# Optimization experiments

Hardware: AMD Instinct MI355X
Metric: run time of the kernel (lower is better)

## Reference

```python
import jax, jax.numpy as jnp
import numpy as np

IMAGE_SIZE = 256
DET = int(IMAGE_SIZE * 2 ** 0.5 + 0.5)  # 362 detector bins (diagonal coverage)
US = 4
N_ACQ = 45                     # acquired views: 0,4,...,176 degrees
N_FULL = (N_ACQ - 1) * US + 1  # 177 full (upsampled) views


def setup_inputs() -> dict:
    key = jax.random.key(0)
    k1, k2 = jax.random.split(key)
    x_source = jax.random.normal(k1, (2, 1, IMAGE_SIZE, IMAGE_SIZE), jnp.float32)
    s_target = jax.random.normal(k2, (2, 1, DET, N_ACQ), jnp.float32)
    theta_acq = np.arange(0, 180, 4, dtype=np.float64)  # 45 acquired angles
    segs = [np.linspace(theta_acq[i], theta_acq[i + 1], US + 1)[:-1] for i in range(N_ACQ - 1)]
    theta_full = np.concatenate(segs + [theta_acq[-1:]]).astype(np.float32)  # [177]
    acq_idx = (np.arange(N_ACQ) * US).astype(np.int32)  # positions of acquired angles in theta_full
    return {"x_source": x_source, "s_target": s_target,
            "thetas_deg": jnp.asarray(theta_full), "acq_idx": jnp.asarray(acq_idx)}


def bilinear_gather(img, xs, ys):
    # img: [B,C,H,W]; xs, ys: pixel coords [A,det,det]; zero outside the image.
    H, W = img.shape[-2], img.shape[-1]
    x0 = jnp.floor(xs); y0 = jnp.floor(ys)
    wx = xs - x0; wy = ys - y0
    x0i = x0.astype(jnp.int32); y0i = y0.astype(jnp.int32)

    def get(yi, xi):
        valid = (xi >= 0) & (xi < W) & (yi >= 0) & (yi < H)
        v = img[:, :, jnp.clip(yi, 0, H - 1), jnp.clip(xi, 0, W - 1)]  # [B,C,A,det,det]
        return jnp.where(valid, v, 0.0)

    return (get(y0i, x0i) * (1 - wy) * (1 - wx)
            + get(y0i, x0i + 1) * (1 - wy) * wx
            + get(y0i + 1, x0i) * wy * (1 - wx)
            + get(y0i + 1, x0i + 1) * wy * wx)


def radon(x, thetas_rad, det):
    # Ray-sum projection: sino[theta, t] = sum_s image(t*cos - s*sin, t*sin + s*cos)
    B, C, H, W = x.shape
    t = jnp.arange(det, dtype=x.dtype) - (det - 1) / 2.0  # centered detector/ray coord
    cos = jnp.cos(thetas_rad)[:, None, None]
    sin = jnp.sin(thetas_rad)[:, None, None]
    T = t[None, :, None]; S = t[None, None, :]
    xs = T * cos - S * sin + (W - 1) / 2.0  # [A,det,det]
    ys = T * sin + S * cos + (H - 1) / 2.0
    return bilinear_gather(x, xs, ys).sum(-1)  # [B,C,A,det]


def ramp_filter(size):
    # skimage/pytorch_radon style ramp built from its real-space kernel
    n = np.concatenate([np.arange(1, size // 2 + 1, 2), np.arange(size // 2 - 1, 0, -2)])
    f = np.zeros(size)
    f[0] = 0.25
    f[1::2] = -1.0 / (np.pi * n) ** 2
    return jnp.asarray(2 * np.real(np.fft.fft(f)), dtype=jnp.float32)


def fbp(sino, thetas_rad, image_size):
    # Filtered back-projection. sino: [B,C,det,A]
    B, C, det, A = sino.shape
    pad = max(64, int(2 ** np.ceil(np.log2(2 * det))))
    filt = ramp_filter(pad)  # [pad]
    sp = jnp.pad(sino, ((0, 0), (0, 0), (0, pad - det), (0, 0)))
    sf = jnp.fft.ifft(jnp.fft.fft(sp, axis=2) * filt[None, None, :, None], axis=2).real
    sf = jnp.transpose(sf[:, :, :det, :], (0, 1, 3, 2)).astype(sino.dtype)  # [B,C,A,det]
    g = jnp.arange(image_size, dtype=sino.dtype) - (image_size - 1) / 2.0
    cos = jnp.cos(thetas_rad); sin = jnp.sin(thetas_rad)
    # detector coordinate hit by each pixel, per angle: t = x*cos + y*sin
    t = (cos[:, None, None] * g[None, None, :]
         + sin[:, None, None] * g[None, :, None] + (det - 1) / 2.0)  # [A,H,W]
    t = t.reshape(A, -1)
    t0 = jnp.floor(t)
    w = t - t0
    t0i = t0.astype(jnp.int32)
    aidx = jnp.arange(A)[:, None]

    def samp(ti):
        valid = (ti >= 0) & (ti < det)
        return jnp.where(valid, sf[:, :, aidx, jnp.clip(ti, 0, det - 1)], 0.0)  # [B,C,A,HW]

    v = samp(t0i) * (1 - w) + samp(t0i + 1) * w
    reco = v.sum(2) * (jnp.pi / (2 * A))
    return reco.reshape(B, C, image_size, image_size)


def reference(x_source, s_target, thetas_deg, acq_idx):
    th = thetas_deg * (jnp.pi / 180.0)
    s = radon(x_source, th, DET)          # [B,C,A,det]
    s = jnp.transpose(s, (0, 1, 3, 2))    # [B,C,det,A] -- angle axis last, as in the module
    # masked data-consistency update: acquired columns become (target - predicted)
    s = s.at[..., acq_idx].set(s_target - s[..., acq_idx])
    return fbp(s, th, IMAGE_SIZE)
```

## Files before the change

### kernel.cpp

```cpp
#include <hip/hip_runtime.h>
#include <math.h>

#define IMG   256
#define NFULL 177
#define DETN  362
#define NACQ  45
#define PAD   1024

#define SINO_OFF 0
#define SF_OFF   131072

#define TTILE  32
#define HALF_T 180.5f
#define SEGL   32
#define TILE_SEG 2548

__constant__ const int kByOrder[12] = {5, 6, 4, 7, 3, 8, 2, 9, 1, 10, 0, 11};

__device__ __forceinline__ void gload16(const float* g, float* l) {
    __builtin_amdgcn_global_load_lds(
        (const __attribute__((address_space(1))) void*)g,
        (__attribute__((address_space(3))) void*)l, 16, 0, 0);
}

template<int P>
__device__ __forceinline__ float radon_core(
    const float* __restrict__ img,
    float* tile,
    const float c, const float s,
    const float xbase, const float ybase,
    const float xAB_mn, const float yAB_mn, const float yAB_mx,
    const int SloB, const int ShiB, const int tid)
{
    constexpr int W4   = P / 4;
    constexpr int HMAX = TILE_SEG / P;
    const int ts   = tid & 7;
    const int wid  = tid >> 6;
    const int lane = tid & 63;

    auto window = [&](int Sseg) -> int4 {
        const float sv0 = (float)Sseg - HALF_T;
        const float sv1 = sv0 + (float)(SEGL - 1);
        const float xmn = xAB_mn - sv1 * s;
        const float ya  = sv0 * c, yb = sv1 * c;
        const float ymn = yAB_mn + fminf(ya, yb);
        const float ymx = yAB_mx + fmaxf(ya, yb);
        const int ix0  = (int)floorf(xmn) - 1;
        const int iy0  = (int)floorf(ymn) - 1;
        const int ix0a = ix0 & ~3;
        const int h    = min((int)floorf(ymx) + 3 - iy0, HMAX);
        const int inter = (ix0a >= 0) & (iy0 >= 0) &
                          (ix0a + P <= IMG) & (iy0 + h <= IMG);
        return make_int4(ix0a, iy0, h, inter);
    };

    auto stage = [&](const int4 wp, float* tb) {
        const int total4 = W4 * wp.z;
        const int nfull  = total4 & ~63;
        if (wp.w) {
            const float* __restrict__ src = img + wp.y * IMG + wp.x;
            for (int f0 = wid * 64; f0 < nfull; f0 += 256) {
                const int f  = f0 + lane;
                const int r  = f / W4;
                const int c4 = f - r * W4;
                gload16(src + r * IMG + (c4 << 2), tb + (f0 << 2));
            }
            const int f = nfull + tid;
            if (f < total4) {
                const int r  = f / W4;
                const int c4 = f - r * W4;
                gload16(src + r * IMG + (c4 << 2), tb + (nfull << 2));
            }
        } else {
            for (int f = tid; f < total4; f += 256) {
                const int r  = f / W4;
                const int c4 = f - r * W4;
                const int gy = wp.y + r;
                const int gx = wp.x + (c4 << 2);
                const bool ok = ((unsigned)gy < (unsigned)IMG) &
                                ((unsigned)gx <= (unsigned)(IMG - 4));
                float4 v = make_float4(0.f, 0.f, 0.f, 0.f);
                if (ok) v = *(const float4*)(img + gy * IMG + gx);
                *(float4*)(tb + (f << 2)) = v;
            }
        }
    };

    float val = 0.0f;
    if (SloB >= ShiB) return val;

    int4 wp = window(SloB);
    stage(wp, tile);
    __syncthreads();

    int cur = 0;
    for (int Sseg = SloB; Sseg < ShiB; Sseg += SEGL) {
        const int Snext = Sseg + SEGL;
        int4 wpn = wp;
        if (Snext < ShiB) {
            wpn = window(Snext);
            stage(wpn, tile + (cur ^ 1) * TILE_SEG);
        }

        const float* __restrict__ tb = tile + cur * TILE_SEG;
        const float xoff = xbase - (float)wp.x;
        const float yoff = ybase - (float)wp.y;
        const int Send = min(Snext, ShiB);

        auto samp = [&](float sval) {
            const float xs  = fmaf(-sval, s, xoff);
            const float ys  = fmaf(sval, c, yoff);
            const float x0f = floorf(xs);
            const float y0f = floorf(ys);
            const float wx  = xs - x0f;
            const float wy  = ys - y0f;
            const int base = (int)fmaf(y0f, (float)P, x0f);
            const float v00 = tb[base];
            const float v01 = tb[base + 1];
            const float v10 = tb[base + P];
            const float v11 = tb[base + P + 1];
            const float h0 = fmaf(wx, v01 - v00, v00);
            const float h1 = fmaf(wx, v11 - v10, v10);
            val += fmaf(wy, h1 - h0, h0);
        };

        if (Send - Sseg == SEGL) {
            const float s0 = (float)(Sseg + ts) - HALF_T;
            #pragma unroll
            for (int u = 0; u < SEGL / 8; ++u) samp(s0 + (float)(8 * u));
        } else {
            for (int S = Sseg + ts; S < Send; S += 8) samp((float)S - HALF_T);
        }
        __syncthreads();
        wp = wpn;
        cur ^= 1;
    }
    return val;
}

__global__ __launch_bounds__(256, 8) void radon_kernel(
    const float* __restrict__ x,
    const float* __restrict__ thetas,
    float* __restrict__ sino)
{
    const int blk = blockIdx.x;
    const int b = blk / NFULL;
    const int a = blk - b * NFULL;
    const int T0 = kByOrder[blockIdx.y] * TTILE;
    const int tid = threadIdx.x;
    const int ts = tid & 7;
    const int tt = tid >> 3;
    const int T = T0 + tt;

    __shared__ __align__(16) float tile[2 * TILE_SEG];
    __shared__ int sRange[2];
    __shared__ int sSel;

    const float th = thetas[a] * (float)(M_PI / 180.0);
    const float c = cosf(th);
    const float s = sinf(th);
    const float cx = (IMG - 1) * 0.5f;
    const float cy = (IMG - 1) * 0.5f;
    const float Tc = (float)T - HALF_T;
    const float xbase = Tc * c + cx;
    const float ybase = Tc * s + cy;

    float lo = -1e30f, hi = 1e30f;
    bool empty = (T >= DETN);
    {   const float aa = -s;
        if (aa > 1e-5f)       { lo = fmaxf(lo, (-1.0f - xbase) / aa); hi = fminf(hi, (256.0f - xbase) / aa); }
        else if (aa < -1e-5f) { lo = fmaxf(lo, (256.0f - xbase) / aa); hi = fminf(hi, (-1.0f - xbase) / aa); }
        else if (xbase <= -1.0f || xbase >= 256.0f) empty = true;
    }
    {   const float aa = c;
        if (aa > 1e-5f)       { lo = fmaxf(lo, (-1.0f - ybase) / aa); hi = fminf(hi, (256.0f - ybase) / aa); }
        else if (aa < -1e-5f) { lo = fmaxf(lo, (256.0f - ybase) / aa); hi = fminf(hi, (-1.0f - ybase) / aa); }
        else if (ybase <= -1.0f || ybase >= 256.0f) empty = true;
    }
    lo = fmaxf(lo, -200.0f);
    hi = fminf(hi, 200.0f);
    int Slo = max(0, (int)floorf(lo + HALF_T) - 1);
    int Shi = min(DETN, (int)floorf(hi + HALF_T) + 2);
    if (empty || Shi < Slo) { Slo = 0; Shi = 0; }

    if (tid == 0) { sRange[0] = DETN; sRange[1] = 0; }
    __syncthreads();
    if (Shi > Slo) { atomicMin(&sRange[0], Slo); atomicMax(&sRange[1], Shi); }

    if (tid < 64) {
        const int ltt = tid >> 3, lts = tid & 7;
        const float ac = fabsf(c), as = fabsf(s);
        const float span = 31.f * (ac + as);
        const int hm[5] = {57, 53, 49, 45, 42};
        int best = 2, bcost = 1 << 30;
        #pragma unroll
        for (int p = 0; p < 5; ++p) {
            const float Pf = 44.f + 4.f * (float)p;
            const float dT = s * Pf + c;
            const float dS = c * Pf - s;
            const int bank = (int)floorf((float)ltt * dT + (float)lts * dS + 0.5f) & 31;
            unsigned long long m = ~0ull;
            #pragma unroll
            for (int bit = 0; bit < 5; ++bit) {
                const unsigned long long bb = __ballot((bank >> bit) & 1);
                m &= ((bank >> bit) & 1) ? bb : ~bb;
            }
            int cnt = __popcll(m);
            #pragma unroll
            for (int d = 1; d < 64; d <<= 1) cnt = max(cnt, __shfl_xor(cnt, d, 64));
            const bool fit = (span <= Pf - 8.05f) && (span <= (float)hm[p] - 5.05f);
            if (fit && cnt < bcost) { bcost = cnt; best = p; }
        }
        if (tid == 0) sSel = best;
    }
    __syncthreads();
    const int SloB = sRange[0], ShiB = sRange[1];
    const int selv = sSel;

    const float TcA = (float)T0 - HALF_T;
    const float TcB = (float)(T0 + TTILE - 1) - HALF_T;
    const float xAB_mn = fminf(TcA * c + cx, TcB * c + cx);
    const float yAB_mn = fminf(TcA * s + cy, TcB * s + cy);
    const float yAB_mx = fmaxf(TcA * s + cy, TcB * s + cy);

    const float* __restrict__ img = x + b * IMG * IMG;

    float val;
    switch (selv) {
    case 0:  val = radon_core<44>(img, tile, c, s, xbase, ybase,
                                  xAB_mn, yAB_mn, yAB_mx, SloB, ShiB, tid); break;
    case 1:  val = radon_core<48>(img, tile, c, s, xbase, ybase,
                                  xAB_mn, yAB_mn, yAB_mx, SloB, ShiB, tid); break;
    case 2:  val = radon_core<52>(img, tile, c, s, xbase, ybase,
                                  xAB_mn, yAB_mn, yAB_mx, SloB, ShiB, tid); break;
    case 3:  val = radon_core<56>(img, tile, c, s, xbase, ybase,
                                  xAB_mn, yAB_mn, yAB_mx, SloB, ShiB, tid); break;
    default: val = radon_core<60>(img, tile, c, s, xbase, ybase,
                                  xAB_mn, yAB_mn, yAB_mx, SloB, ShiB, tid); break;
    }

    val += __shfl_xor(val, 1, 8);
    val += __shfl_xor(val, 2, 8);
    val += __shfl_xor(val, 4, 8);
    if (ts == 0 && T < DETN) {
        sino[(b * NFULL + a) * DETN + T] = val;
    }
}

__global__ __launch_bounds__(192) void dc_filter_kernel(
    const float* __restrict__ sino,
    const float* __restrict__ st,
    const int*   __restrict__ acq,
    float* __restrict__ sf)
{
    const int blk = blockIdx.x;
    const int b = blk / NFULL;
    const int a = blk - b * NFULL;
    const int tid = threadIdx.x;

    __shared__ float col[DETN];
    __shared__ float gf[PAD];

    const float SC = (float)(M_PI / (2.0 * NFULL));
    const float c0 = 0.5f * SC;
    for (int n = tid; n < PAD; n += 192) {
        float v = 0.0f;
        if (n & 1) {
            const int d = (n < PAD - n) ? n : (PAD - n);
            const float pd = (float)M_PI * (float)d;
            v = -2.0f / (pd * pd) * SC;
        }
        gf[n] = v;
    }

    int inv = -1;
    for (int i = 0; i < NACQ; ++i) {
        if (acq[i] == a) inv = i;
    }

    for (int m = tid; m < DETN; m += 192) {
        float val = sino[(b * NFULL + a) * DETN + m];
        if (inv >= 0) {
            val = st[(b * DETN + m) * NACQ + inv] - val;
        }
        col[m] = val;
    }
    __syncthreads();

    const int T = blockIdx.y * 181 + tid;
    if (tid < 181) {
        const int m0 = (T + 1) & 1;
        float acc = c0 * col[T];
        #pragma unroll 4
        for (int k = 0; k < 181; ++k) {
            const int m = m0 + 2 * k;
            acc += col[m] * gf[(T - m) & (PAD - 1)];
        }
        sf[(b * NFULL + a) * DETN + T] = acc;
    }
}

__global__ __launch_bounds__(256) void backproject_kernel(
    const float* __restrict__ sf,
    const float* __restrict__ thetas,
    float* __restrict__ out)
{
    __shared__ float cb[2 * NFULL];
    __shared__ float red[256];
    const int tid = threadIdx.x;
    const int lane  = tid & 63;
    const int phase = tid >> 6;
    const int pix = blockIdx.x * 64 + lane;
    const int b = pix >> 16;
    const int y = (pix >> 8) & 255;
    const int xq = pix & 255;
    const float gx = (float)xq - (IMG - 1) * 0.5f;
    const float gy = (float)y  - (IMG - 1) * 0.5f;

    for (int a = tid; a < NFULL; a += 256) {
        float th = thetas[a] * (float)(M_PI / 180.0);
        cb[2 * a]     = cosf(th);
        cb[2 * a + 1] = fmaf(sinf(th), gy, HALF_T);
    }
    __syncthreads();

    const float* __restrict__ sfb = sf + b * NFULL * DETN;

    float acc = 0.0f;
    #pragma unroll 4
    for (int a = phase; a < NFULL; a += 4) {
        const float cs = cb[2 * a];
        const float bs = cb[2 * a + 1];
        const float t = fmaf(cs, gx, bs);
        const float t0f = floorf(t);
        const float w = t - t0f;
        const float* row = sfb + a * DETN + (int)t0f;
        const float v0 = row[0];
        const float v1 = row[1];
        acc += v0 + w * (v1 - v0);
    }
    red[tid] = acc;
    __syncthreads();
    if (tid < 64) {
        out[blockIdx.x * 64 + tid] =
            red[tid] + red[tid + 64] + red[tid + 128] + red[tid + 192];
    }
}

extern "C" void kernel_launch(void* const* d_in, const int* in_sizes, int n_in,
                              void* d_out, int out_size, void* d_ws, size_t ws_size,
                              hipStream_t stream) {
    const float* x      = (const float*)d_in[0];
    const float* st     = (const float*)d_in[1];
    const float* thetas = (const float*)d_in[2];
    const int*   acq    = (const int*)d_in[3];
    float* out  = (float*)d_out;
    float* wsf  = (float*)d_ws;
    float* sino = wsf + SINO_OFF;
    float* sf   = wsf + SF_OFF;

    dim3 gA(2 * NFULL, 12);
    radon_kernel<<<gA, 256, 0, stream>>>(x, thetas, sino);
    dim3 gB(2 * NFULL, 2);
    dc_filter_kernel<<<gB, 192, 0, stream>>>(sino, st, acq, sf);
    backproject_kernel<<<(2 * IMG * IMG) / 64, 256, 0, stream>>>(sf, thetas, out);
}
```

Measured before the change: 126.8 us.

## Restructure radon kernel into per-wave 8-detector strips with wave-local LDS staging

```diff
diff --git a/kernel.cpp b/kernel.cpp
--- a/kernel.cpp
+++ b/kernel.cpp
@@ -10,12 +10,12 @@
 #define SINO_OFF 0
 #define SF_OFF   131072
 
-#define TTILE  32
 #define HALF_T 180.5f
 #define SEGL   32
-#define TILE_SEG 2548
-
-__constant__ const int kByOrder[12] = {5, 6, 4, 7, 3, 8, 2, 9, 1, 10, 0, 11};
+#define TILE_W 1276
+
+__constant__ const int kPairOrd[23] =
+    {11,10,12,9,13,8,14,7,15,6,16,5,17,4,18,3,19,2,20,1,21,0,22};
 
 __device__ __forceinline__ void gload16(const float* g, float* l) {
     __builtin_amdgcn_global_load_lds(
@@ -24,21 +24,20 @@
 }
 
 template<int P>
-__device__ __forceinline__ float radon_core(
+__device__ __forceinline__ float radon_strip(
     const float* __restrict__ img,
-    float* tile,
+    float* tb,
     const float c, const float s,
     const float xbase, const float ybase,
     const float xAB_mn, const float yAB_mn, const float yAB_mx,
-    const int SloB, const int ShiB, const int tid)
+    const int Slo, const int Shi, const int lane)
 {
     constexpr int W4   = P / 4;
-    constexpr int HMAX = TILE_SEG / P;
-    const int ts   = tid & 7;
-    const int wid  = tid >> 6;
-    const int lane = tid & 63;
-
-    auto window = [&](int Sseg) -> int4 {
+    constexpr int HMAX = TILE_W / P;
+    const int ts = lane & 7;
+    float val = 0.0f;
+
+    for (int Sseg = Slo; Sseg < Shi; Sseg += SEGL) {
         const float sv0 = (float)Sseg - HALF_T;
         const float sv1 = sv0 + (float)(SEGL - 1);
         const float xmn = xAB_mn - sv1 * s;
@@ -49,34 +48,33 @@
         const int iy0  = (int)floorf(ymn) - 1;
         const int ix0a = ix0 & ~3;
         const int h    = min((int)floorf(ymx) + 3 - iy0, HMAX);
-        const int inter = (ix0a >= 0) & (iy0 >= 0) &
-                          (ix0a + P <= IMG) & (iy0 + h <= IMG);
-        return make_int4(ix0a, iy0, h, inter);
-    };
-
-    auto stage = [&](const int4 wp, float* tb) {
-        const int total4 = W4 * wp.z;
+        const int total4 = W4 * h;
         const int nfull  = total4 & ~63;
-        if (wp.w) {
-            const float* __restrict__ src = img + wp.y * IMG + wp.x;
-            for (int f0 = wid * 64; f0 < nfull; f0 += 256) {
+        const bool interior = (ix0a >= 0) & (iy0 >= 0) &
+                              (ix0a + P <= IMG) & (iy0 + h <= IMG);
+
+        asm volatile("s_waitcnt lgkmcnt(0)" ::: "memory");
+
+        if (interior) {
+            const float* __restrict__ src = img + iy0 * IMG + ix0a;
+            for (int f0 = 0; f0 < nfull; f0 += 64) {
                 const int f  = f0 + lane;
                 const int r  = f / W4;
                 const int c4 = f - r * W4;
                 gload16(src + r * IMG + (c4 << 2), tb + (f0 << 2));
             }
-            const int f = nfull + tid;
+            const int f = nfull + lane;
             if (f < total4) {
                 const int r  = f / W4;
                 const int c4 = f - r * W4;
                 gload16(src + r * IMG + (c4 << 2), tb + (nfull << 2));
             }
         } else {
-            for (int f = tid; f < total4; f += 256) {
+            for (int f = lane; f < total4; f += 64) {
                 const int r  = f / W4;
                 const int c4 = f - r * W4;
-                const int gy = wp.y + r;
-                const int gx = wp.x + (c4 << 2);
+                const int gy = iy0 + r;
+                const int gx = ix0a + (c4 << 2);
                 const bool ok = ((unsigned)gy < (unsigned)IMG) &
                                 ((unsigned)gx <= (unsigned)(IMG - 4));
                 float4 v = make_float4(0.f, 0.f, 0.f, 0.f);
@@ -84,28 +82,12 @@
                 *(float4*)(tb + (f << 2)) = v;
             }
         }
-    };
-
-    float val = 0.0f;
-    if (SloB >= ShiB) return val;
-
-    int4 wp = window(SloB);
-    stage(wp, tile);
-    __syncthreads();
-
-    int cur = 0;
-    for (int Sseg = SloB; Sseg < ShiB; Sseg += SEGL) {
-        const int Snext = Sseg + SEGL;
-        int4 wpn = wp;
-        if (Snext < ShiB) {
-            wpn = window(Snext);
-            stage(wpn, tile + (cur ^ 1) * TILE_SEG);
-        }
-
-        const float* __restrict__ tb = tile + cur * TILE_SEG;
-        const float xoff = xbase - (float)wp.x;
-        const float yoff = ybase - (float)wp.y;
-        const int Send = min(Snext, ShiB);
+        asm volatile("s_waitcnt vmcnt(0) lgkmcnt(0)" ::: "memory");
+        __builtin_amdgcn_sched_barrier(0);
+
+        const float xoff = xbase - (float)ix0a;
+        const float yoff = ybase - (float)iy0;
+        const int Send = min(Sseg + SEGL, Shi);
 
         auto samp = [&](float sval) {
             const float xs  = fmaf(-sval, s, xoff);
@@ -131,14 +113,11 @@
         } else {
             for (int S = Sseg + ts; S < Send; S += 8) samp((float)S - HALF_T);
         }
-        __syncthreads();
-        wp = wpn;
-        cur ^= 1;
     }
     return val;
 }
 
-__global__ __launch_bounds__(256, 8) void radon_kernel(
+__global__ __launch_bounds__(128, 8) void radon_kernel(
     const float* __restrict__ x,
     const float* __restrict__ thetas,
     float* __restrict__ sino)
@@ -146,15 +125,16 @@
     const int blk = blockIdx.x;
     const int b = blk / NFULL;
     const int a = blk - b * NFULL;
-    const int T0 = kByOrder[blockIdx.y] * TTILE;
-    const int tid = threadIdx.x;
-    const int ts = tid & 7;
-    const int tt = tid >> 3;
-    const int T = T0 + tt;
-
-    __shared__ __align__(16) float tile[2 * TILE_SEG];
-    __shared__ int sRange[2];
-    __shared__ int sSel;
+    const int w    = threadIdx.x >> 6;
+    const int lane = threadIdx.x & 63;
+    const int sp   = kPairOrd[blockIdx.y] * 2 + w;
+    const int T0   = sp << 3;
+    const int tt   = lane >> 3;
+    const int ts   = lane & 7;
+    const int T    = T0 + tt;
+
+    __shared__ __align__(16) float tile[2][TILE_W];
+    float* tb = tile[w];
 
     const float th = thetas[a] * (float)(M_PI / 180.0);
     const float c = cosf(th);
@@ -183,22 +163,28 @@
     int Shi = min(DETN, (int)floorf(hi + HALF_T) + 2);
     if (empty || Shi < Slo) { Slo = 0; Shi = 0; }
 
-    if (tid == 0) { sRange[0] = DETN; sRange[1] = 0; }
-    __syncthreads();
-    if (Shi > Slo) { atomicMin(&sRange[0], Slo); atomicMax(&sRange[1], Shi); }
-
-    if (tid < 64) {
-        const int ltt = tid >> 3, lts = tid & 7;
+    int wlo = (Shi > Slo) ? Slo : DETN;
+    int whi = (Shi > Slo) ? Shi : 0;
+    #pragma unroll
+    for (int d = 1; d < 64; d <<= 1) {
+        wlo = min(wlo, __shfl_xor(wlo, d, 64));
+        whi = max(whi, __shfl_xor(whi, d, 64));
+    }
+
+    int best = 2;
+    {
         const float ac = fabsf(c), as = fabsf(s);
-        const float span = 31.f * (ac + as);
-        const int hm[5] = {57, 53, 49, 45, 42};
-        int best = 2, bcost = 1 << 30;
+        const float spanx = 7.f * ac + 31.f * as;
+        const float spany = 7.f * as + 31.f * ac;
+        const float Pc[6] = {16.f, 24.f, 32.f, 36.f, 40.f, 44.f};
+        const int   Hm[6] = {79, 53, 39, 35, 31, 29};
+        int bcost = 1 << 30;
         #pragma unroll
-        for (int p = 0; p < 5; ++p) {
-            const float Pf = 44.f + 4.f * (float)p;
+        for (int p = 0; p < 6; ++p) {
+            const float Pf = Pc[p];
             const float dT = s * Pf + c;
             const float dS = c * Pf - s;
-            const int bank = (int)floorf((float)ltt * dT + (float)lts * dS + 0.5f) & 31;
+            const int bank = (int)floorf((float)tt * dT + (float)ts * dS + 0.5f) & 31;
             unsigned long long m = ~0ull;
             #pragma unroll
             for (int bit = 0; bit < 5; ++bit) {
@@ -208,17 +194,13 @@
             int cnt = __popcll(m);
             #pragma unroll
             for (int d = 1; d < 64; d <<= 1) cnt = max(cnt, __shfl_xor(cnt, d, 64));
-            const bool fit = (span <= Pf - 8.05f) && (span <= (float)hm[p] - 5.05f);
+            const bool fit = (spanx <= Pf - 8.05f) && (spany <= (float)Hm[p] - 5.05f);
             if (fit && cnt < bcost) { bcost = cnt; best = p; }
         }
-        if (tid == 0) sSel = best;
-    }
-    __syncthreads();
-    const int SloB = sRange[0], ShiB = sRange[1];
-    const int selv = sSel;
+    }
 
     const float TcA = (float)T0 - HALF_T;
-    const float TcB = (float)(T0 + TTILE - 1) - HALF_T;
+    const float TcB = (float)(T0 + 7) - HALF_T;
     const float xAB_mn = fminf(TcA * c + cx, TcB * c + cx);
     const float yAB_mn = fminf(TcA * s + cy, TcB * s + cy);
     const float yAB_mx = fmaxf(TcA * s + cy, TcB * s + cy);
@@ -226,17 +208,19 @@
     const float* __restrict__ img = x + b * IMG * IMG;
 
     float val;
-    switch (selv) {
-    case 0:  val = radon_core<44>(img, tile, c, s, xbase, ybase,
-                                  xAB_mn, yAB_mn, yAB_mx, SloB, ShiB, tid); break;
-    case 1:  val = radon_core<48>(img, tile, c, s, xbase, ybase,
-                                  xAB_mn, yAB_mn, yAB_mx, SloB, ShiB, tid); break;
-    case 2:  val = radon_core<52>(img, tile, c, s, xbase, ybase,
-                                  xAB_mn, yAB_mn, yAB_mx, SloB, ShiB, tid); break;
-    case 3:  val = radon_core<56>(img, tile, c, s, xbase, ybase,
-                                  xAB_mn, yAB_mn, yAB_mx, SloB, ShiB, tid); break;
-    default: val = radon_core<60>(img, tile, c, s, xbase, ybase,
-                                  xAB_mn, yAB_mn, yAB_mx, SloB, ShiB, tid); break;
+    switch (best) {
+    case 0:  val = radon_strip<16>(img, tb, c, s, xbase, ybase,
+                                   xAB_mn, yAB_mn, yAB_mx, wlo, whi, lane); break;
+    case 1:  val = radon_strip<24>(img, tb, c, s, xbase, ybase,
+                                   xAB_mn, yAB_mn, yAB_mx, wlo, whi, lane); break;
+    case 2:  val = radon_strip<32>(img, tb, c, s, xbase, ybase,
+                                   xAB_mn, yAB_mn, yAB_mx, wlo, whi, lane); break;
+    case 3:  val = radon_strip<36>(img, tb, c, s, xbase, ybase,
+                                   xAB_mn, yAB_mn, yAB_mx, wlo, whi, lane); break;
+    case 4:  val = radon_strip<40>(img, tb, c, s, xbase, ybase,
+                                   xAB_mn, yAB_mn, yAB_mx, wlo, whi, lane); break;
+    default: val = radon_strip<44>(img, tb, c, s, xbase, ybase,
+                                   xAB_mn, yAB_mn, yAB_mx, wlo, whi, lane); break;
     }
 
     val += __shfl_xor(val, 1, 8);
@@ -359,8 +343,8 @@
     float* sino = wsf + SINO_OFF;
     float* sf   = wsf + SF_OFF;
 
-    dim3 gA(2 * NFULL, 12);
-    radon_kernel<<<gA, 256, 0, stream>>>(x, thetas, sino);
+    dim3 gA(2 * NFULL, 23);
+    radon_kernel<<<gA, 128, 0, stream>>>(x, thetas, sino);
     dim3 gB(2 * NFULL, 2);
     dc_filter_kernel<<<gB, 192, 0, stream>>>(sino, st, acq, sf);
     backproject_kernel<<<(2 * IMG * IMG) / 64, 256, 0, stream>>>(sf, thetas, out);
```

Measured after the change: 121.5 us. 1.04x faster.
